# Optimization experiments

Hardware: AMD Instinct MI355X
Metric: run time of the kernel (lower is better)

## Reference

```python
import jax, jax.numpy as jnp
import numpy as np
import math

L, D, H, FF = 6, 512, 8, 2048
B, S = 8, 1024
EPS = 1e-5


def sin_pos_embedding(num_embeddings, dim, padding_idx=0):
    half = dim // 2
    freq = jnp.exp(jnp.arange(half, dtype=jnp.float32) * (-math.log(10000.0) / (half - 1)))
    ang = jnp.arange(num_embeddings, dtype=jnp.float32)[:, None] * freq[None, :]
    emb = jnp.concatenate([jnp.sin(ang), jnp.cos(ang)], axis=1)
    return emb.at[padding_idx].set(0.0)


def layer_norm(x, g, b):
    mu = jnp.mean(x, axis=-1, keepdims=True)
    var = jnp.mean(jnp.square(x - mu), axis=-1, keepdims=True)
    return (x - mu) * jax.lax.rsqrt(var + EPS) * g + b


def setup_inputs() -> dict:
    key = jax.random.key(0)
    ks = jax.random.split(key, 16)
    s = 0.02
    inp = {
        'x': jax.random.normal(ks[0], (B, S, D), jnp.float32),
        'char_ids': jax.random.randint(ks[1], (B, S), 0, 10000, jnp.int64) if jax.config.read('jax_enable_x64') else jax.random.randint(ks[1], (B, S), 0, 10000, jnp.int32),
        'seq_len': jnp.full((B,), S, jnp.int32),
        'mask': jnp.ones((B, S), jnp.int32),
        'Wqkv': jax.random.normal(ks[2], (L, D, 3 * D), jnp.float32) * s,
        'Wfc': jax.random.normal(ks[3], (L, D, D), jnp.float32) * s,
        'bfc': jnp.zeros((L, D), jnp.float32),
        'ln1_g': jnp.ones((L, D), jnp.float32), 'ln1_b': jnp.zeros((L, D), jnp.float32),
        'ln2_g': jnp.ones((L, D), jnp.float32), 'ln2_b': jnp.zeros((L, D), jnp.float32),
        'W1': jax.random.normal(ks[4], (L, D, FF), jnp.float32) * s,
        'b1': jnp.zeros((L, FF), jnp.float32),
        'W2': jax.random.normal(ks[5], (L, FF, D), jnp.float32) * s,
        'b2': jnp.zeros((L, D), jnp.float32),
    }
    return inp


def reference(x, char_ids, seq_len, mask, Wqkv, Wfc, bfc, ln1_g, ln1_b, ln2_g, ln2_b, W1, b1, W2, b2):
    # sinusoidal positional embedding computed from mask positions (padding_idx=0)
    valid = (mask != 0).astype(jnp.int32)
    positions = jnp.cumsum(valid, axis=1) * valid  # [B,S], pads -> 0
    table = sin_pos_embedding(S + 2, D)  # max_pos = padding_idx+1+S
    x = x + table[positions]

    key_mask = (mask == 0)[:, None, None, :]  # [B,1,1,S]
    dh = D // H

    for l in range(L):
        residual = x
        qkv = jnp.einsum('bsd,de->bse', x, Wqkv[l])  # [B,S,3D]
        q, k, v = jnp.split(qkv, 3, axis=-1)
        q = q.reshape(B, S, H, dh).transpose(0, 2, 1, 3)  # [B,H,S,dh]
        k = k.reshape(B, S, H, dh).transpose(0, 2, 1, 3)
        v = v.reshape(B, S, H, dh).transpose(0, 2, 1, 3)
        attn = jnp.einsum('bhqd,bhkd->bhqk', q, k)  # scale=1 (scale=False)
        attn = jnp.where(key_mask, -jnp.inf, attn)
        attn = jax.nn.softmax(attn, axis=-1)
        o = jnp.einsum('bhqk,bhkd->bhqd', attn, v)
        o = o.transpose(0, 2, 1, 3).reshape(B, S, D)
        o = jnp.einsum('bsd,de->bse', o, Wfc[l]) + bfc[l]
        x = layer_norm(o + residual, ln1_g[l], ln1_b[l])
        residual = x
        h = jax.nn.relu(jnp.einsum('bsd,df->bsf', x, W1[l]) + b1[l])
        h = jnp.einsum('bsf,fd->bsd', h, W2[l]) + b2[l]
        x = layer_norm(residual + h, ln2_g[l], ln2_b[l])
    return x
```

## Files before the change

### kernel.cpp

```cpp
#include <hip/hip_runtime.h>
#include <math.h>

#define LAYERS 6
#define DMODEL 512
#define NHEAD 8
#define DHEAD 64
#define FFDIM 2048
#define BATCH 8
#define SEQ 1024
#define ROWS (BATCH * SEQ)
#define EPS 1e-5f

typedef __attribute__((ext_vector_type(8))) short bf16x8;
typedef __attribute__((ext_vector_type(4))) float f32x4;
typedef __attribute__((ext_vector_type(16))) float f32x16;

__device__ inline short f2bf(float f) {
    union { float f; unsigned u; } v; v.f = f;
    unsigned r = (v.u + 0x7FFFu + ((v.u >> 16) & 1u)) >> 16;
    return (short)r;
}

#define GLOAD_LDS16(g, l)                                                      \
    __builtin_amdgcn_global_load_lds(                                          \
        (__attribute__((address_space(1))) void*)(g),                          \
        (__attribute__((address_space(3))) void*)(l), 16, 0, 0)

__global__ void wtrans_kernel(const float* __restrict__ src, short* __restrict__ dst,
                              int K, int N) {
    __shared__ float t[32][33];
    const size_t mofs = (size_t)blockIdx.z * K * N;
    src += mofs; dst += mofs;
    int n0 = blockIdx.x * 32, k0 = blockIdx.y * 32;
    int tx = threadIdx.x, ty = threadIdx.y;
#pragma unroll
    for (int i = 0; i < 4; ++i)
        t[ty + 8 * i][tx] = src[(size_t)(k0 + ty + 8 * i) * N + n0 + tx];
    __syncthreads();
#pragma unroll
    for (int i = 0; i < 4; ++i)
        dst[(size_t)(n0 + ty + 8 * i) * K + k0 + tx] = f2bf(t[tx][ty + 8 * i]);
}

__global__ void pos_scan_kernel(const int* __restrict__ mask, int* __restrict__ pos) {
    __shared__ int sm[SEQ];
    int b = blockIdx.x;
    int t = threadIdx.x;
    int v = (mask[b * SEQ + t] != 0) ? 1 : 0;
    sm[t] = v;
    __syncthreads();
    for (int off = 1; off < SEQ; off <<= 1) {
        int add = (t >= off) ? sm[t - off] : 0;
        __syncthreads();
        sm[t] += add;
        __syncthreads();
    }
    pos[b * SEQ + t] = sm[t] * v;
}

__global__ void add_pos_kernel(const float* __restrict__ xin, const int* __restrict__ pos,
                               float* __restrict__ xout, short* __restrict__ xb) {
    int bs = blockIdx.x;
    int t = threadIdx.x;
    int p = pos[bs];
    int d0 = t * 4;
    const float C = -logf(10000.0f) * (1.0f / 255.0f);
    float4 xv = *(const float4*)(xin + (size_t)bs * DMODEL + d0);
    float e[4];
#pragma unroll
    for (int j = 0; j < 4; ++j) {
        int d = d0 + j;
        if (p == 0) {
            e[j] = 0.0f;
        } else {
            int dd = (d < 256) ? d : d - 256;
            float freq = expf((float)dd * C);
            float ang = (float)p * freq;
            e[j] = (d < 256) ? sinf(ang) : cosf(ang);
        }
    }
    float4 ov;
    ov.x = xv.x + e[0]; ov.y = xv.y + e[1]; ov.z = xv.z + e[2]; ov.w = xv.w + e[3];
    *(float4*)(xout + (size_t)bs * DMODEL + d0) = ov;
    short4 sb;
    sb.x = f2bf(ov.x); sb.y = f2bf(ov.y); sb.z = f2bf(ov.z); sb.w = f2bf(ov.w);
    *(short4*)(xb + (size_t)bs * DMODEL + d0) = sb;
}


template <bool OUTBF16, bool BIAS, bool RELU>
__global__ __launch_bounds__(256) void gemm_bf16_kernel(const short* __restrict__ A,
                                                        const short* __restrict__ BT,
                                                        const float* __restrict__ bias,
                                                        void* __restrict__ Cv,
                                                        int M, int N, int K) {
    __shared__ __attribute__((aligned(16))) short Asm[2][128 * 32];
    __shared__ __attribute__((aligned(16))) short Bsm[2][128 * 32];
    const int tid = threadIdx.x;
    const int w = tid >> 6;
    const int lane = tid & 63;
    const int quad = lane >> 4;
    const int lr = lane & 15;
    const int m0 = blockIdx.y * 128;
    const int n0 = blockIdx.x * 128;
    const int wm = (w >> 1) * 64;
    const int wn = (w & 1) * 64;

    const int segr = lane >> 2;
    const int segk = (((lane & 3) - (lane >> 3)) & 3) * 8;
    const int sA0 = w * 2, sA1 = w * 2 + 1;
    const short* gA0 = A + (size_t)(m0 + sA0 * 16 + segr) * K + segk;
    const short* gA1 = A + (size_t)(m0 + sA1 * 16 + segr) * K + segk;
    const short* gB0 = BT + (size_t)(n0 + sA0 * 16 + segr) * K + segk;
    const short* gB1 = BT + (size_t)(n0 + sA1 * 16 + segr) * K + segk;
    const int lofs0 = sA0 * 512 + lane * 8;
    const int lofs1 = sA1 * 512 + lane * 8;
    const int gp = ((quad + (lr >> 1)) & 3) * 8;

    f32x4 acc[4][4];
#pragma unroll
    for (int i = 0; i < 4; ++i)
#pragma unroll
        for (int j = 0; j < 4; ++j) { acc[i][j][0] = 0.f; acc[i][j][1] = 0.f; acc[i][j][2] = 0.f; acc[i][j][3] = 0.f; }

    GLOAD_LDS16(gA0, &Asm[0][lofs0]);
    GLOAD_LDS16(gA1, &Asm[0][lofs1]);
    GLOAD_LDS16(gB0, &Bsm[0][lofs0]);
    GLOAD_LDS16(gB1, &Bsm[0][lofs1]);

    const int nk = K >> 5;
    for (int i = 0; i < nk; ++i) {
        __syncthreads();
        if (i + 1 < nk) {
            const int k1 = (i + 1) * 32;
            const int nb = (i + 1) & 1;
            GLOAD_LDS16(gA0 + k1, &Asm[nb][lofs0]);
            GLOAD_LDS16(gA1 + k1, &Asm[nb][lofs1]);
            GLOAD_LDS16(gB0 + k1, &Bsm[nb][lofs0]);
            GLOAD_LDS16(gB1 + k1, &Bsm[nb][lofs1]);
        }
        const int cur = i & 1;
        bf16x8 af[4], bfr[4];
#pragma unroll
        for (int mt = 0; mt < 4; ++mt)
            af[mt] = *(const bf16x8*)&Asm[cur][(wm + mt * 16 + lr) * 32 + gp];
#pragma unroll
        for (int nt = 0; nt < 4; ++nt)
            bfr[nt] = *(const bf16x8*)&Bsm[cur][(wn + nt * 16 + lr) * 32 + gp];
#pragma unroll
        for (int mt = 0; mt < 4; ++mt)
#pragma unroll
            for (int nt = 0; nt < 4; ++nt)
                acc[mt][nt] = __builtin_amdgcn_mfma_f32_16x16x32_bf16(af[mt], bfr[nt], acc[mt][nt], 0, 0, 0);
    }

    float bv[4];
    if (BIAS) {
#pragma unroll
        for (int nt = 0; nt < 4; ++nt) bv[nt] = bias[n0 + wn + nt * 16 + lr];
    }
#pragma unroll
    for (int mt = 0; mt < 4; ++mt)
#pragma unroll
        for (int nt = 0; nt < 4; ++nt)
#pragma unroll
            for (int r = 0; r < 4; ++r) {
                float v = acc[mt][nt][r];
                if (BIAS) v += bv[nt];
                if (RELU) v = fmaxf(v, 0.f);
                int row = m0 + wm + mt * 16 + quad * 4 + r;
                int col = n0 + wn + nt * 16 + lr;
                if (OUTBF16)
                    ((short*)Cv)[(size_t)row * N + col] = f2bf(v);
                else
                    ((float*)Cv)[(size_t)row * N + col] = v;
            }
}

template <bool OUTBF16, bool BIAS, bool RELU>
__global__ __launch_bounds__(256) void gemm_bf16_m64_kernel(const short* __restrict__ A,
                                                            const short* __restrict__ BT,
                                                            const float* __restrict__ bias,
                                                            void* __restrict__ Cv,
                                                            int M, int N, int K) {
    __shared__ __attribute__((aligned(16))) short Asm[2][64 * 32];
    __shared__ __attribute__((aligned(16))) short Bsm[2][128 * 32];
    const int tid = threadIdx.x;
    const int w = tid >> 6;
    const int lane = tid & 63;
    const int quad = lane >> 4;
    const int lr = lane & 15;
    const int m0 = blockIdx.y * 64;
    const int n0 = blockIdx.x * 128;
    const int wm = (w >> 1) * 32;
    const int wn = (w & 1) * 64;

    const int segr = lane >> 2;
    const int segk = (((lane & 3) - (lane >> 3)) & 3) * 8;
    const short* gA  = A + (size_t)(m0 + w * 16 + segr) * K + segk;
    const short* gB0 = BT + (size_t)(n0 + (2 * w) * 16 + segr) * K + segk;
    const short* gB1 = BT + (size_t)(n0 + (2 * w + 1) * 16 + segr) * K + segk;
    const int lA  = w * 512 + lane * 8;
    const int lB0 = (2 * w) * 512 + lane * 8;
    const int lB1 = (2 * w + 1) * 512 + lane * 8;
    const int gp = ((quad + (lr >> 1)) & 3) * 8;

    f32x4 acc[2][4];
#pragma unroll
    for (int i = 0; i < 2; ++i)
#pragma unroll
        for (int j = 0; j < 4; ++j) { acc[i][j][0] = 0.f; acc[i][j][1] = 0.f; acc[i][j][2] = 0.f; acc[i][j][3] = 0.f; }

    GLOAD_LDS16(gA, &Asm[0][lA]);
    GLOAD_LDS16(gB0, &Bsm[0][lB0]);
    GLOAD_LDS16(gB1, &Bsm[0][lB1]);

    const int nk = K >> 5;
    for (int i = 0; i < nk; ++i) {
        __syncthreads();
        if (i + 1 < nk) {
            const int k1 = (i + 1) * 32;
            const int nb = (i + 1) & 1;
            GLOAD_LDS16(gA + k1, &Asm[nb][lA]);
            GLOAD_LDS16(gB0 + k1, &Bsm[nb][lB0]);
            GLOAD_LDS16(gB1 + k1, &Bsm[nb][lB1]);
        }
        const int cur = i & 1;
        bf16x8 af[2], bfr[4];
#pragma unroll
        for (int mt = 0; mt < 2; ++mt)
            af[mt] = *(const bf16x8*)&Asm[cur][(wm + mt * 16 + lr) * 32 + gp];
#pragma unroll
        for (int nt = 0; nt < 4; ++nt)
            bfr[nt] = *(const bf16x8*)&Bsm[cur][(wn + nt * 16 + lr) * 32 + gp];
#pragma unroll
        for (int mt = 0; mt < 2; ++mt)
#pragma unroll
            for (int nt = 0; nt < 4; ++nt)
                acc[mt][nt] = __builtin_amdgcn_mfma_f32_16x16x32_bf16(af[mt], bfr[nt], acc[mt][nt], 0, 0, 0);
    }

    float bv[4];
    if (BIAS) {
#pragma unroll
        for (int nt = 0; nt < 4; ++nt) bv[nt] = bias[n0 + wn + nt * 16 + lr];
    }
#pragma unroll
    for (int mt = 0; mt < 2; ++mt)
#pragma unroll
        for (int nt = 0; nt < 4; ++nt)
#pragma unroll
            for (int r = 0; r < 4; ++r) {
                float v = acc[mt][nt][r];
                if (BIAS) v += bv[nt];
                if (RELU) v = fmaxf(v, 0.f);
                int row = m0 + wm + mt * 16 + quad * 4 + r;
                int col = n0 + wn + nt * 16 + lr;
                if (OUTBF16)
                    ((short*)Cv)[(size_t)row * N + col] = f2bf(v);
                else
                    ((float*)Cv)[(size_t)row * N + col] = v;
            }
}

#define QTILE 256
__global__ __launch_bounds__(512, 2) void attn_mfma_kernel(const short* __restrict__ qkv,
                                                           const int* __restrict__ mask,
                                                           short* __restrict__ o) {
    __shared__ __attribute__((aligned(16))) short Ks[2][64][72];
    __shared__ __attribute__((aligned(16))) short Vt[2][64][72];
    __shared__ __attribute__((aligned(16))) float Msf[2][64];

    const int qt = blockIdx.x;
    const int bh = blockIdx.y;
    const int b = bh >> 3, h = bh & 7;
    const int tid = threadIdx.x;
    const int w = tid >> 6;
    const int lane = tid & 63;
    const int c31 = lane & 31;
    const int hi = lane >> 5;
    const size_t seqrow = (size_t)b * SEQ;

    bf16x8 qf[4];
#pragma unroll
    for (int ks = 0; ks < 4; ++ks)
        qf[ks] = *(const bf16x8*)(qkv +
            (seqrow + qt * QTILE + w * 32 + c31) * (3 * DMODEL)
            + h * DHEAD + ks * 16 + hi * 8);

    const bool isK = (tid < 256);
    const int st = isK ? tid : tid - 256;
    const int kkey = st >> 2;
    const int kg = (st & 3) * 8;
    const int vkp = st & 31;
    const int vdg = st >> 5;
    const short* gK = qkv + (seqrow + kkey) * (3 * DMODEL) + DMODEL + h * DHEAD + kg;
    const short* gV = qkv + (seqrow + 2 * vkp) * (3 * DMODEL) + 2 * DMODEL + h * DHEAD + vdg * 8;

    bf16x8 r0, r1;
    int mreg = 0;

    {
        if (isK) {
            r0 = *(const bf16x8*)(gK);
            r1 = *(const bf16x8*)(gK + 32);
        } else {
            r0 = *(const bf16x8*)(gV);
            r1 = *(const bf16x8*)(gV + 3 * DMODEL);
        }
        if (tid < 64) mreg = mask[seqrow + tid];
        if (isK) {
            *(bf16x8*)&Ks[0][kkey][kg] = r0;
            *(bf16x8*)&Ks[0][kkey][kg + 32] = r1;
        } else {
#pragma unroll
            for (int i = 0; i < 8; ++i) {
                short2 p; p.x = r0[i]; p.y = r1[i];
                *(short2*)&Vt[0][vdg * 8 + i][vkp * 2] = p;
            }
        }
        if (tid < 64) Msf[0][tid] = mreg ? 1.0f : 0.0f;
    }
    __syncthreads();

    f32x16 O0, O1;
    float rs = 0.f;
#pragma unroll
    for (int i = 0; i < 16; ++i) { O0[i] = 0.f; O1[i] = 0.f; }

    for (int kt = 0; kt < 16; ++kt) {
        const int cur = kt & 1;
        {
            const size_t ofs = (size_t)((kt + 1) & 15) * 64 * (3 * DMODEL);
            if (isK) {
                r0 = *(const bf16x8*)(gK + ofs);
                r1 = *(const bf16x8*)(gK + ofs + 32);
            } else {
                r0 = *(const bf16x8*)(gV + ofs);
                r1 = *(const bf16x8*)(gV + ofs + 3 * DMODEL);
            }
            if (tid < 64) mreg = mask[seqrow + ((kt + 1) & 15) * 64 + tid];
        }

        f32x16 S0, S1;
#pragma unroll
        for (int i = 0; i < 16; ++i) { S0[i] = 0.f; S1[i] = 0.f; }
#pragma unroll
        for (int ks = 0; ks < 4; ++ks) {
            bf16x8 k0 = *(const bf16x8*)&Ks[cur][c31][ks * 16 + hi * 8];
            bf16x8 k1 = *(const bf16x8*)&Ks[cur][32 + c31][ks * 16 + hi * 8];
            S0 = __builtin_amdgcn_mfma_f32_32x32x16_bf16(k0, qf[ks], S0, 0, 0, 0);
            S1 = __builtin_amdgcn_mfma_f32_32x32x16_bf16(k1, qf[ks], S1, 0, 0, 0);
        }

        unsigned pkd[2][8];
#pragma unroll
        for (int g = 0; g < 4; ++g) {
            f32x4 m0 = *(const f32x4*)&Msf[cur][g * 8 + hi * 4];
            f32x4 m1 = *(const f32x4*)&Msf[cur][32 + g * 8 + hi * 4];
            float p0[4], p1[4];
#pragma unroll
            for (int j = 0; j < 4; ++j) {
                p0[j] = __expf(S0[g * 4 + j] - 8.0f) * m0[j];
                p1[j] = __expf(S1[g * 4 + j] - 8.0f) * m1[j];
                rs += p0[j] + p1[j];
            }
            asm("v_cvt_pk_bf16_f32 %0, %1, %2" : "=v"(pkd[0][g * 2])     : "v"(p0[0]), "v"(p0[1]));
            asm("v_cvt_pk_bf16_f32 %0, %1, %2" : "=v"(pkd[0][g * 2 + 1]) : "v"(p0[2]), "v"(p0[3]));
            asm("v_cvt_pk_bf16_f32 %0, %1, %2" : "=v"(pkd[1][g * 2])     : "v"(p1[0]), "v"(p1[1]));
            asm("v_cvt_pk_bf16_f32 %0, %1, %2" : "=v"(pkd[1][g * 2 + 1]) : "v"(p1[2]), "v"(p1[3]));
        }

#pragma unroll
        for (int ks = 0; ks < 4; ++ks) {
            const int k2 = ks >> 1;
            const int i0 = (ks & 1) * 4;
            unsigned c0a = pkd[k2][i0 + 0], c0b = pkd[k2][i0 + 1];
            unsigned c1a = pkd[k2][i0 + 2], c1b = pkd[k2][i0 + 3];
            unsigned x1a = (unsigned)__shfl_xor((int)c1a, 32);
            unsigned x1b = (unsigned)__shfl_xor((int)c1b, 32);
            unsigned x0a = (unsigned)__shfl_xor((int)c0a, 32);
            unsigned x0b = (unsigned)__shfl_xor((int)c0b, 32);
            union { unsigned u[4]; bf16x8 v; } pb;
            pb.u[0] = hi ? x1a : c0a;
            pb.u[1] = hi ? x1b : c0b;
            pb.u[2] = hi ? c1a : x0a;
            pb.u[3] = hi ? c1b : x0b;
            bf16x8 v0 = *(const bf16x8*)&Vt[cur][c31][ks * 16 + hi * 8];
            bf16x8 v1 = *(const bf16x8*)&Vt[cur][32 + c31][ks * 16 + hi * 8];
            O0 = __builtin_amdgcn_mfma_f32_32x32x16_bf16(pb.v, v0, O0, 0, 0, 0);
            O1 = __builtin_amdgcn_mfma_f32_32x32x16_bf16(pb.v, v1, O1, 0, 0, 0);
        }

        {
            const int nb = cur ^ 1;
            if (isK) {
                *(bf16x8*)&Ks[nb][kkey][kg] = r0;
                *(bf16x8*)&Ks[nb][kkey][kg + 32] = r1;
            } else {
#pragma unroll
                for (int i = 0; i < 8; ++i) {
                    short2 p; p.x = r0[i]; p.y = r1[i];
                    *(short2*)&Vt[nb][vdg * 8 + i][vkp * 2] = p;
                }
            }
            if (tid < 64) Msf[nb][tid] = mreg ? 1.0f : 0.0f;
        }
        __syncthreads();
    }

    rs += __shfl_xor(rs, 32);

#pragma unroll
    for (int r = 0; r < 16; ++r) {
        const int qr = (r & 3) + 8 * (r >> 2) + 4 * hi;
        const float inv = 1.0f / __shfl(rs, qr);
        const int row = qt * QTILE + w * 32 + qr;
        o[(seqrow + row) * DMODEL + h * DHEAD + c31]      = f2bf(O0[r] * inv);
        o[(seqrow + row) * DMODEL + h * DHEAD + 32 + c31] = f2bf(O1[r] * inv);
    }
}

__global__ __launch_bounds__(64) void ln_kernel(const float* __restrict__ tmp,
                                                float* __restrict__ x,
                                                short* __restrict__ xb,
                                                const float* __restrict__ g,
                                                const float* __restrict__ bta) {
    const int row = blockIdx.x;
    const int t = threadIdx.x;
    const size_t base = (size_t)row * DMODEL + t * 8;
    float4 x0 = *(const float4*)(x + base);
    float4 x1 = *(const float4*)(x + base + 4);
    float4 t0 = *(const float4*)(tmp + base);
    float4 t1 = *(const float4*)(tmp + base + 4);
    float v[8];
    v[0] = x0.x + t0.x; v[1] = x0.y + t0.y; v[2] = x0.z + t0.z; v[3] = x0.w + t0.w;
    v[4] = x1.x + t1.x; v[5] = x1.y + t1.y; v[6] = x1.z + t1.z; v[7] = x1.w + t1.w;
    float s = 0.f, sq = 0.f;
#pragma unroll
    for (int i = 0; i < 8; ++i) { s += v[i]; sq += v[i] * v[i]; }
#pragma unroll
    for (int off = 1; off < 64; off <<= 1) {
        s += __shfl_xor(s, off);
        sq += __shfl_xor(sq, off);
    }
    float mu = s * (1.0f / DMODEL);
    float var = sq * (1.0f / DMODEL) - mu * mu;
    float r = rsqrtf(var + EPS);
    float4 g0 = *(const float4*)(g + t * 8);
    float4 g1 = *(const float4*)(g + t * 8 + 4);
    float4 b0 = *(const float4*)(bta + t * 8);
    float4 b1 = *(const float4*)(bta + t * 8 + 4);
    float ov[8];
    ov[0] = (v[0] - mu) * r * g0.x + b0.x;
    ov[1] = (v[1] - mu) * r * g0.y + b0.y;
    ov[2] = (v[2] - mu) * r * g0.z + b0.z;
    ov[3] = (v[3] - mu) * r * g0.w + b0.w;
    ov[4] = (v[4] - mu) * r * g1.x + b1.x;
    ov[5] = (v[5] - mu) * r * g1.y + b1.y;
    ov[6] = (v[6] - mu) * r * g1.z + b1.z;
    ov[7] = (v[7] - mu) * r * g1.w + b1.w;
    *(float4*)(x + base) = *(float4*)&ov[0];
    *(float4*)(x + base + 4) = *(float4*)&ov[4];
    bf16x8 ob;
#pragma unroll
    for (int i = 0; i < 8; ++i) ob[i] = f2bf(ov[i]);
    *(bf16x8*)(xb + base) = ob;
}

extern "C" void kernel_launch(void* const* d_in, const int* in_sizes, int n_in,
                              void* d_out, int out_size, void* d_ws, size_t ws_size,
                              hipStream_t stream) {
    const float* x_in  = (const float*)d_in[0];
    const int*   mask  = (const int*)d_in[3];
    const float* Wqkv  = (const float*)d_in[4];
    const float* Wfc   = (const float*)d_in[5];
    const float* bfc   = (const float*)d_in[6];
    const float* ln1_g = (const float*)d_in[7];
    const float* ln1_b = (const float*)d_in[8];
    const float* ln2_g = (const float*)d_in[9];
    const float* ln2_b = (const float*)d_in[10];
    const float* W1    = (const float*)d_in[11];
    const float* b1    = (const float*)d_in[12];
    const float* W2    = (const float*)d_in[13];
    const float* b2    = (const float*)d_in[14];

    float* x = (float*)d_out;

    char* ws = (char*)d_ws;
    size_t ofs = 0;
    int*   pos   = (int*)ws;                 ofs += 65536;
    float* tmp   = (float*)(ws + ofs);       ofs += (size_t)ROWS * DMODEL * 4;
    short* xb    = (short*)(ws + ofs);       ofs += (size_t)ROWS * DMODEL * 2;
    short* qkvb  = (short*)(ws + ofs);
    short* hb    = (short*)(ws + ofs);
    ofs += (size_t)ROWS * 3 * DMODEL * 2;
    short* obuf  = (short*)(ws + ofs);       ofs += (size_t)ROWS * DMODEL * 2;
    short* WqkvT = (short*)(ws + ofs);       ofs += (size_t)LAYERS * DMODEL * 3 * DMODEL * 2;
    short* WfcT  = (short*)(ws + ofs);       ofs += (size_t)LAYERS * DMODEL * DMODEL * 2;
    short* W1T   = (short*)(ws + ofs);       ofs += (size_t)LAYERS * DMODEL * FFDIM * 2;
    short* W2T   = (short*)(ws + ofs);       ofs += (size_t)LAYERS * FFDIM * DMODEL * 2;

    wtrans_kernel<<<dim3(3 * DMODEL / 32, DMODEL / 32, LAYERS), dim3(32, 8), 0, stream>>>(
        Wqkv, WqkvT, DMODEL, 3 * DMODEL);
    wtrans_kernel<<<dim3(DMODEL / 32, DMODEL / 32, LAYERS), dim3(32, 8), 0, stream>>>(
        Wfc, WfcT, DMODEL, DMODEL);
    wtrans_kernel<<<dim3(FFDIM / 32, DMODEL / 32, LAYERS), dim3(32, 8), 0, stream>>>(
        W1, W1T, DMODEL, FFDIM);
    wtrans_kernel<<<dim3(DMODEL / 32, FFDIM / 32, LAYERS), dim3(32, 8), 0, stream>>>(
        W2, W2T, FFDIM, DMODEL);

    pos_scan_kernel<<<BATCH, SEQ, 0, stream>>>(mask, pos);
    add_pos_kernel<<<ROWS, 128, 0, stream>>>(x_in, pos, x, xb);

    for (int l = 0; l < LAYERS; ++l) {
        const short* wqkvT_l = WqkvT + (size_t)l * DMODEL * 3 * DMODEL;
        const short* wfcT_l  = WfcT + (size_t)l * DMODEL * DMODEL;
        const short* w1T_l   = W1T + (size_t)l * DMODEL * FFDIM;
        const short* w2T_l   = W2T + (size_t)l * FFDIM * DMODEL;
        const float* bfc_l   = bfc + (size_t)l * DMODEL;
        const float* b1_l    = b1 + (size_t)l * FFDIM;
        const float* b2_l    = b2 + (size_t)l * DMODEL;

        gemm_bf16_kernel<true, false, false><<<dim3(3 * DMODEL / 128, ROWS / 128), 256, 0, stream>>>(
            xb, wqkvT_l, nullptr, qkvb, ROWS, 3 * DMODEL, DMODEL);
        attn_mfma_kernel<<<dim3(SEQ / QTILE, BATCH * NHEAD), 512, 0, stream>>>(qkvb, mask, obuf);
        gemm_bf16_m64_kernel<false, true, false><<<dim3(DMODEL / 128, ROWS / 64), 256, 0, stream>>>(
            obuf, wfcT_l, bfc_l, tmp, ROWS, DMODEL, DMODEL);
        ln_kernel<<<ROWS, 64, 0, stream>>>(tmp, x, xb, ln1_g + (size_t)l * DMODEL,
                                           ln1_b + (size_t)l * DMODEL);
        gemm_bf16_kernel<true, true, true><<<dim3(FFDIM / 128, ROWS / 128), 256, 0, stream>>>(
            xb, w1T_l, b1_l, hb, ROWS, FFDIM, DMODEL);
        gemm_bf16_m64_kernel<false, true, false><<<dim3(DMODEL / 128, ROWS / 64), 256, 0, stream>>>(
            hb, w2T_l, b2_l, tmp, ROWS, DMODEL, FFDIM);
        ln_kernel<<<ROWS, 64, 0, stream>>>(tmp, x, xb, ln2_g + (size_t)l * DMODEL,
                                           ln2_b + (size_t)l * DMODEL);
    }
}
```

Before: 1.091 ms.

## Add XCD block swizzle, setprio around MFMAs, K64 tiles in m64 GEMM, additive mask

Several independent changes land together. Both GEMM kernels remap block IDs so consecutive blocks on the same XCD share nearby tiles for L2 reuse, and MFMA loops are wrapped in s_setprio to favour matrix issue. The m64 GEMM now stages two 32-wide K slices per barrier, which halves the number of syncs at the cost of double the LDS use. The attention kernel folds the mask into an additive bias (-8 or -1e30) inside exp, removing one multiply per element.

```diff
diff --git a/kernel.cpp b/kernel.cpp
--- a/kernel.cpp
+++ b/kernel.cpp
@@ -25,6 +25,14 @@
     __builtin_amdgcn_global_load_lds(                                          \
         (__attribute__((address_space(1))) void*)(g),                          \
         (__attribute__((address_space(3))) void*)(l), 16, 0, 0)
+
+#define XCD_SWIZZLE(TM)                                                        \
+    const int gx_ = gridDim.x;                                                 \
+    const int bid_ = blockIdx.x + gx_ * blockIdx.y;                            \
+    const int chunk_ = (gx_ * gridDim.y) >> 3;                                 \
+    const int nb_ = (bid_ & 7) * chunk_ + (bid_ >> 3);                         \
+    const int m0 = (nb_ / gx_) * (TM);                                         \
+    const int n0 = (nb_ % gx_) * 128;
 
 __global__ void wtrans_kernel(const float* __restrict__ src, short* __restrict__ dst,
                               int K, int N) {
@@ -101,8 +109,7 @@
     const int lane = tid & 63;
     const int quad = lane >> 4;
     const int lr = lane & 15;
-    const int m0 = blockIdx.y * 128;
-    const int n0 = blockIdx.x * 128;
+    XCD_SWIZZLE(128)
     const int wm = (w >> 1) * 64;
     const int wn = (w & 1) * 64;
 
@@ -147,11 +154,13 @@
 #pragma unroll
         for (int nt = 0; nt < 4; ++nt)
             bfr[nt] = *(const bf16x8*)&Bsm[cur][(wn + nt * 16 + lr) * 32 + gp];
+        __builtin_amdgcn_s_setprio(1);
 #pragma unroll
         for (int mt = 0; mt < 4; ++mt)
 #pragma unroll
             for (int nt = 0; nt < 4; ++nt)
                 acc[mt][nt] = __builtin_amdgcn_mfma_f32_16x16x32_bf16(af[mt], bfr[nt], acc[mt][nt], 0, 0, 0);
+        __builtin_amdgcn_s_setprio(0);
     }
 
     float bv[4];
@@ -183,15 +192,14 @@
                                                             const float* __restrict__ bias,
                                                             void* __restrict__ Cv,
                                                             int M, int N, int K) {
-    __shared__ __attribute__((aligned(16))) short Asm[2][64 * 32];
-    __shared__ __attribute__((aligned(16))) short Bsm[2][128 * 32];
+    __shared__ __attribute__((aligned(16))) short Asm[2][2][64 * 32];
+    __shared__ __attribute__((aligned(16))) short Bsm[2][2][128 * 32];
     const int tid = threadIdx.x;
     const int w = tid >> 6;
     const int lane = tid & 63;
     const int quad = lane >> 4;
     const int lr = lane & 15;
-    const int m0 = blockIdx.y * 64;
-    const int n0 = blockIdx.x * 128;
+    XCD_SWIZZLE(64)
     const int wm = (w >> 1) * 32;
     const int wn = (w & 1) * 64;
 
@@ -211,33 +219,44 @@
 #pragma unroll
         for (int j = 0; j < 4; ++j) { acc[i][j][0] = 0.f; acc[i][j][1] = 0.f; acc[i][j][2] = 0.f; acc[i][j][3] = 0.f; }
 
-    GLOAD_LDS16(gA, &Asm[0][lA]);
-    GLOAD_LDS16(gB0, &Bsm[0][lB0]);
-    GLOAD_LDS16(gB1, &Bsm[0][lB1]);
-
-    const int nk = K >> 5;
+#pragma unroll
+    for (int kh = 0; kh < 2; ++kh) {
+        GLOAD_LDS16(gA + kh * 32, &Asm[0][kh][lA]);
+        GLOAD_LDS16(gB0 + kh * 32, &Bsm[0][kh][lB0]);
+        GLOAD_LDS16(gB1 + kh * 32, &Bsm[0][kh][lB1]);
+    }
+
+    const int nk = K >> 6;
     for (int i = 0; i < nk; ++i) {
         __syncthreads();
         if (i + 1 < nk) {
-            const int k1 = (i + 1) * 32;
+            const int k1 = (i + 1) * 64;
             const int nb = (i + 1) & 1;
-            GLOAD_LDS16(gA + k1, &Asm[nb][lA]);
-            GLOAD_LDS16(gB0 + k1, &Bsm[nb][lB0]);
-            GLOAD_LDS16(gB1 + k1, &Bsm[nb][lB1]);
+#pragma unroll
+            for (int kh = 0; kh < 2; ++kh) {
+                GLOAD_LDS16(gA + k1 + kh * 32, &Asm[nb][kh][lA]);
+                GLOAD_LDS16(gB0 + k1 + kh * 32, &Bsm[nb][kh][lB0]);
+                GLOAD_LDS16(gB1 + k1 + kh * 32, &Bsm[nb][kh][lB1]);
+            }
         }
         const int cur = i & 1;
-        bf16x8 af[2], bfr[4];
-#pragma unroll
-        for (int mt = 0; mt < 2; ++mt)
-            af[mt] = *(const bf16x8*)&Asm[cur][(wm + mt * 16 + lr) * 32 + gp];
-#pragma unroll
-        for (int nt = 0; nt < 4; ++nt)
-            bfr[nt] = *(const bf16x8*)&Bsm[cur][(wn + nt * 16 + lr) * 32 + gp];
-#pragma unroll
-        for (int mt = 0; mt < 2; ++mt)
+#pragma unroll
+        for (int kh = 0; kh < 2; ++kh) {
+            bf16x8 af[2], bfr[4];
+#pragma unroll
+            for (int mt = 0; mt < 2; ++mt)
+                af[mt] = *(const bf16x8*)&Asm[cur][kh][(wm + mt * 16 + lr) * 32 + gp];
 #pragma unroll
             for (int nt = 0; nt < 4; ++nt)
-                acc[mt][nt] = __builtin_amdgcn_mfma_f32_16x16x32_bf16(af[mt], bfr[nt], acc[mt][nt], 0, 0, 0);
+                bfr[nt] = *(const bf16x8*)&Bsm[cur][kh][(wn + nt * 16 + lr) * 32 + gp];
+            __builtin_amdgcn_s_setprio(1);
+#pragma unroll
+            for (int mt = 0; mt < 2; ++mt)
+#pragma unroll
+                for (int nt = 0; nt < 4; ++nt)
+                    acc[mt][nt] = __builtin_amdgcn_mfma_f32_16x16x32_bf16(af[mt], bfr[nt], acc[mt][nt], 0, 0, 0);
+            __builtin_amdgcn_s_setprio(0);
+        }
     }
 
     float bv[4];
@@ -319,7 +338,7 @@
                 *(short2*)&Vt[0][vdg * 8 + i][vkp * 2] = p;
             }
         }
-        if (tid < 64) Msf[0][tid] = mreg ? 1.0f : 0.0f;
+        if (tid < 64) Msf[0][tid] = mreg ? -8.0f : -1e30f;
     }
     __syncthreads();
 
@@ -345,6 +364,7 @@
         f32x16 S0, S1;
 #pragma unroll
         for (int i = 0; i < 16; ++i) { S0[i] = 0.f; S1[i] = 0.f; }
+        __builtin_amdgcn_s_setprio(1);
 #pragma unroll
         for (int ks = 0; ks < 4; ++ks) {
             bf16x8 k0 = *(const bf16x8*)&Ks[cur][c31][ks * 16 + hi * 8];
@@ -352,6 +372,7 @@
             S0 = __builtin_amdgcn_mfma_f32_32x32x16_bf16(k0, qf[ks], S0, 0, 0, 0);
             S1 = __builtin_amdgcn_mfma_f32_32x32x16_bf16(k1, qf[ks], S1, 0, 0, 0);
         }
+        __builtin_amdgcn_s_setprio(0);
 
         unsigned pkd[2][8];
 #pragma unroll
@@ -361,8 +382,8 @@
             float p0[4], p1[4];
 #pragma unroll
             for (int j = 0; j < 4; ++j) {
-                p0[j] = __expf(S0[g * 4 + j] - 8.0f) * m0[j];
-                p1[j] = __expf(S1[g * 4 + j] - 8.0f) * m1[j];
+                p0[j] = __expf(S0[g * 4 + j] + m0[j]);
+                p1[j] = __expf(S1[g * 4 + j] + m1[j]);
                 rs += p0[j] + p1[j];
             }
             asm("v_cvt_pk_bf16_f32 %0, %1, %2" : "=v"(pkd[0][g * 2])     : "v"(p0[0]), "v"(p0[1]));
@@ -388,8 +409,10 @@
             pb.u[3] = hi ? c1b : x0b;
             bf16x8 v0 = *(const bf16x8*)&Vt[cur][c31][ks * 16 + hi * 8];
             bf16x8 v1 = *(const bf16x8*)&Vt[cur][32 + c31][ks * 16 + hi * 8];
+            __builtin_amdgcn_s_setprio(1);
             O0 = __builtin_amdgcn_mfma_f32_32x32x16_bf16(pb.v, v0, O0, 0, 0, 0);
             O1 = __builtin_amdgcn_mfma_f32_32x32x16_bf16(pb.v, v1, O1, 0, 0, 0);
+            __builtin_amdgcn_s_setprio(0);
         }
 
         {
@@ -404,7 +427,7 @@
                     *(short2*)&Vt[nb][vdg * 8 + i][vkp * 2] = p;
                 }
             }
-            if (tid < 64) Msf[nb][tid] = mreg ? 1.0f : 0.0f;
+            if (tid < 64) Msf[nb][tid] = mreg ? -8.0f : -1e30f;
         }
         __syncthreads();
     }
```

After: 1.004 ms. 1.09x faster.
